# Kernel optimization log

Measured on AMD Instinct MI355X. Metric: run time of the kernel, lower is better.

The kernel has to match this reference:

```python
import jax, jax.numpy as jnp
import numpy as np

CAPS = 16          # num_capsules
DIM = 16           # capsule_dim
NUM_ROUTING = 3
L2_EPS = 1e-12     # tf.nn.l2_normalize epsilon


def setup_inputs() -> dict:
    key = jax.random.key(0)
    k1, k2 = jax.random.split(key)
    inputs = jax.random.normal(k1, (16, 64, 64, 128), dtype=jnp.float32)
    # Conv2D kernel, HWIO layout, fan-in scaled like glorot-ish init
    kernel = jax.random.normal(k2, (3, 3, 128, CAPS * DIM), dtype=jnp.float32) * 0.03
    bias = jnp.zeros((CAPS * DIM,), dtype=jnp.float32)
    return {"inputs": inputs, "kernel": kernel, "bias": bias}


def reference(inputs, kernel, bias):
    # Conv2D(caps*dim, 3x3, padding='same', activation='relu'), channels_last
    x = jax.lax.conv_general_dilated(
        inputs, kernel, window_strides=(1, 1), padding="SAME",
        dimension_numbers=("NHWC", "HWIO", "NHWC"))
    x = jax.nn.relu(x + bias)
    B, H, W, _ = x.shape
    x = x.reshape(B, H * W, CAPS, DIM)            # (B, N, C, D)
    b = jnp.zeros((B, H * W, CAPS), dtype=x.dtype)
    v = None
    for _ in range(NUM_ROUTING):
        c = jax.nn.softmax(b, axis=-1)             # over capsules
        s = jnp.einsum("bnc,bncd->bcd", c, x)      # weighted sum over spatial
        # tf.nn.l2_normalize along last axis
        v = s * jax.lax.rsqrt(jnp.maximum(jnp.sum(s * s, axis=-1, keepdims=True), L2_EPS))
        b = b + jnp.einsum("bncd,bcd->bnc", x, v)  # agreement update
    # tile v over spatial dims: (B,1,1,C*D) -> (B,H,W,C*D)
    out = jnp.broadcast_to(v.reshape(B, 1, 1, CAPS * DIM), (B, H, W, CAPS * DIM))
    return out
```

## Files before the change

### kernel.cpp

```cpp
#include <hip/hip_runtime.h>
#include <hip/hip_bf16.h>

typedef unsigned short u16;
typedef unsigned int   u32;

typedef __bf16 bf16x8 __attribute__((ext_vector_type(8)));
typedef float  f32x4  __attribute__((ext_vector_type(4)));

__device__ __forceinline__ u16 f2b(float f) {
    __hip_bfloat16 h = __float2bfloat16(f);
    u16 u; __builtin_memcpy(&u, &h, 2); return u;
}
__device__ __forceinline__ float blo(u32 u) { return __uint_as_float(u << 16); }
__device__ __forceinline__ float bhi(u32 u) { return __uint_as_float(u & 0xffff0000u); }

__global__ void k_prep(const float* __restrict__ wk,
                       u16* __restrict__ BF, float* __restrict__ stats) {
    int bx = blockIdx.x, tid = threadIdx.x;
    if (bx < 1152) {
        int t = bx * 256 + tid;
        int j  = t & 7;
        int n  = (t >> 3) & 255;
        int q  = (t >> 11) & 3;
        int kk = (t >> 13) & 3;
        int p  = t >> 15;
        BF[t] = f2b(wk[(p * 128 + kk * 32 + q * 8 + j) * 256 + n]);
    } else {
        stats[(bx - 1152) * 256 + tid] = 0.f;
    }
}

__launch_bounds__(256, 2)
__global__ void k_conv(const float* __restrict__ in, const u16* __restrict__ BF,
                       const float* __restrict__ bias,
                       u16* __restrict__ X, float* __restrict__ s0) {
    __shared__ u16 ldsA[12672];
    const int t = threadIdx.x;
    const int lane = t & 63, wid = t >> 6;
    const int q = lane >> 4, l15 = lane & 15;
    const int bb = blockIdx.x >> 6;
    const int h  = blockIdx.x & 63;
    const int wn0 = wid << 6;

#define STAGE(S) { \
    const int sb0 = wid * 396; \
    _Pragma("unroll") for (int i = 0; i < 7; ++i) { \
        int slot = sb0 + i * 64 + lane; \
        if (i < 6 || lane < 12) { \
            int pr = slot / 528; int rem = slot - pr * 528; \
            int wp = rem >> 3, cs = rem & 7; \
            int gc = (S) * 8 + (cs ^ (wp & 7)); \
            int y = h + pr - 1, x = wp - 1; \
            u16 ov[8]; \
            if (y >= 0 && y < 64 && x >= 0 && x < 64) { \
                const float4* s4 = (const float4*)(in + \
                    (((bb * 64 + y) * 64 + x) * 128 + gc * 8)); \
                float4 f0 = s4[0], f1 = s4[1]; \
                ov[0]=f2b(f0.x); ov[1]=f2b(f0.y); ov[2]=f2b(f0.z); ov[3]=f2b(f0.w); \
                ov[4]=f2b(f1.x); ov[5]=f2b(f1.y); ov[6]=f2b(f1.z); ov[7]=f2b(f1.w); \
            } else { \
                _Pragma("unroll") for (int j = 0; j < 8; ++j) ov[j] = 0; \
            } \
            uint4 wv; __builtin_memcpy(&wv, ov, 16); \
            *(uint4*)((char*)ldsA + slot * 16) = wv; \
        } \
    } }

#define LOADB(B, P, S) { \
    _Pragma("unroll") for (int kk = 0; kk < 2; ++kk) \
    _Pragma("unroll") for (int ni = 0; ni < 4; ++ni) \
        B[kk * 4 + ni] = *(const bf16x8*)(BFl + (P) * 32768 + \
                                          ((S) * 2 + kk) * 8192 + ni * 128); }

#define COMPP(B, DH, DW) { \
    _Pragma("unroll") for (int kk = 0; kk < 2; ++kk) { \
        bf16x8 af[4]; \
        _Pragma("unroll") for (int mi = 0; mi < 4; ++mi) { \
            int wp = mi * 16 + l15 + (DW); \
            int swz = (kk * 4 + q) ^ (wp & 7); \
            af[mi] = *(const bf16x8*)((const char*)ldsA + \
                (((DH) * 528 + wp * 8 + swz) << 4)); \
        } \
        _Pragma("unroll") for (int mi = 0; mi < 4; ++mi) \
        _Pragma("unroll") for (int ni = 0; ni < 4; ++ni) \
            acc[mi][ni] = __builtin_amdgcn_mfma_f32_16x16x32_bf16( \
                af[mi], B[kk * 4 + ni], acc[mi][ni], 0, 0, 0); } }

    const u16* BFl = BF + (q * 2048 + (wn0 + l15) * 8);

    f32x4 zero = {0.f, 0.f, 0.f, 0.f};
    f32x4 acc[4][4];
    #pragma unroll
    for (int mi = 0; mi < 4; ++mi)
        #pragma unroll
        for (int ni = 0; ni < 4; ++ni) acc[mi][ni] = zero;

    bf16x8 B0[8], B1[8];

    STAGE(0);
    __syncthreads();
    LOADB(B0, 0, 0);
    LOADB(B1, 1, 0); COMPP(B0, 0, 0);
    LOADB(B0, 2, 0); COMPP(B1, 0, 1);
    LOADB(B1, 3, 0); COMPP(B0, 0, 2);
    LOADB(B0, 4, 0); COMPP(B1, 1, 0);
    LOADB(B1, 5, 0); COMPP(B0, 1, 1);
    LOADB(B0, 6, 0); COMPP(B1, 1, 2);
    LOADB(B1, 7, 0); COMPP(B0, 2, 0);
    LOADB(B0, 8, 0); COMPP(B1, 2, 1);
    COMPP(B0, 2, 2);
    __syncthreads();

    STAGE(1);
    __syncthreads();
    LOADB(B0, 0, 1);
    LOADB(B1, 1, 1); COMPP(B0, 0, 0);
    LOADB(B0, 2, 1); COMPP(B1, 0, 1);
    LOADB(B1, 3, 1); COMPP(B0, 0, 2);
    LOADB(B0, 4, 1); COMPP(B1, 1, 0);
    LOADB(B1, 5, 1); COMPP(B0, 1, 1);
    LOADB(B0, 6, 1); COMPP(B1, 1, 2);
    LOADB(B1, 7, 1); COMPP(B0, 2, 0);
    LOADB(B0, 8, 1); COMPP(B1, 2, 1);
    COMPP(B0, 2, 2);

    float bv[4];
    #pragma unroll
    for (int ni = 0; ni < 4; ++ni) bv[ni] = bias[wn0 + ni * 16 + l15];
    float colsum[4] = {0.f, 0.f, 0.f, 0.f};
    u16* xrow = X + (((bb << 12) + (h << 6) + q * 4) * 256) + wn0 + l15;
    #pragma unroll
    for (int mi = 0; mi < 4; ++mi) {
        #pragma unroll
        for (int rr = 0; rr < 4; ++rr) {
            u16* xp = xrow + (mi * 16 + rr) * 256;
            #pragma unroll
            for (int ni = 0; ni < 4; ++ni) {
                float v = acc[mi][ni][rr] + bv[ni];
                v = v > 0.f ? v : 0.f;
                xp[ni * 16] = f2b(v);
                colsum[ni] += v;
            }
        }
    }
    #pragma unroll
    for (int ni = 0; ni < 4; ++ni) {
        float c = colsum[ni];
        c += __shfl_xor(c, 16);
        c += __shfl_xor(c, 32);
        if (lane < 16) atomicAdd(&s0[bb * 256 + wn0 + ni * 16 + l15], c);
    }
#undef STAGE
#undef LOADB
#undef COMPP
}

__launch_bounds__(256, 4)
__global__ void k_pass(const u16* __restrict__ X, const float* __restrict__ Sa,
                       const float* __restrict__ Sb, float* __restrict__ Sout,
                       int use2) {
    __shared__ float vs[272];
    __shared__ float red[4 * 272];
    const int t = threadIdx.x, b = blockIdx.y, chunk = blockIdx.x;
    const int c = t & 15, nl = t >> 4;
    const int lane = t & 63, wid = t >> 6;
    {
        float sa = Sa[b * 256 + t];
        float ss = sa * sa;
        #pragma unroll
        for (int off = 1; off < 16; off <<= 1) ss += __shfl_xor(ss, off);
        ss = ss < 1e-12f ? 1e-12f : ss;
        float vv = sa / sqrtf(ss);
        if (use2) {
            float sb = Sb[b * 256 + t];
            float s2v = sb * sb;
            #pragma unroll
            for (int off = 1; off < 16; off <<= 1) s2v += __shfl_xor(s2v, off);
            s2v = s2v < 1e-12f ? 1e-12f : s2v;
            vv += sb / sqrtf(s2v);
        }
        vs[(t >> 4) * 17 + (t & 15)] = vv;
    }
    const u16* xbase = X + ((b << 12) + chunk * 64 + nl) * 256 + c * 16;
    uint4 pa[8];
    #pragma unroll
    for (int r = 0; r < 4; ++r) {
        pa[2 * r]     = ((const uint4*)(xbase + r * 4096))[0];
        pa[2 * r + 1] = ((const uint4*)(xbase + r * 4096))[1];
    }
    __syncthreads();
    float vr[16];
    #pragma unroll
    for (int d = 0; d < 16; ++d) vr[d] = vs[c * 17 + d];

    float acc[16];
    #pragma unroll
    for (int d = 0; d < 16; ++d) acc[d] = 0.f;

    #pragma unroll
    for (int r = 0; r < 4; ++r) {
        u32 us[8];
        __builtin_memcpy(us, &pa[2 * r], 32);
        float xf[16];
        #pragma unroll
        for (int j = 0; j < 8; ++j) { xf[2*j] = blo(us[j]); xf[2*j+1] = bhi(us[j]); }
        float bvv = 0.f;
        #pragma unroll
        for (int d = 0; d < 16; ++d) bvv += xf[d] * vr[d];
        float e = __expf(bvv);
        float sm = e;
        #pragma unroll
        for (int off = 1; off < 16; off <<= 1) sm += __shfl_xor(sm, off);
        float w = e / sm;
        #pragma unroll
        for (int d = 0; d < 16; ++d) acc[d] += w * xf[d];
    }
    #pragma unroll
    for (int d = 0; d < 16; ++d) {
        acc[d] += __shfl_xor(acc[d], 16);
        acc[d] += __shfl_xor(acc[d], 32);
    }
    if (lane < 16) {
        #pragma unroll
        for (int d = 0; d < 16; ++d) red[wid * 272 + lane * 17 + d] = acc[d];
    }
    __syncthreads();
    {
        int c2 = t >> 4, d2 = t & 15;
        float tot = red[c2 * 17 + d2]       + red[272 + c2 * 17 + d2]
                  + red[544 + c2 * 17 + d2] + red[816 + c2 * 17 + d2];
        atomicAdd(&Sout[b * 256 + t], tot);
    }
}

__launch_bounds__(256, 4)
__global__ void k_bcast(const float* __restrict__ S, float* __restrict__ Out) {
    __shared__ float vls[256];
    int t = threadIdx.x, bx = blockIdx.x, b = blockIdx.y;
    float s = S[b * 256 + t];
    float ss = s * s;
    #pragma unroll
    for (int off = 1; off < 16; off <<= 1) ss += __shfl_xor(ss, off);
    ss = ss < 1e-12f ? 1e-12f : ss;
    vls[t] = s / sqrtf(ss);
    __syncthreads();
    float4 myv = ((const float4*)vls)[t & 63];
    float4* o = (float4*)Out + (long)b * 262144 + bx * 4096;
    #pragma unroll
    for (int j = 0; j < 16; ++j) o[j * 256 + t] = myv;
}

extern "C" void kernel_launch(void* const* d_in, const int* in_sizes, int n_in,
                              void* d_out, int out_size, void* d_ws, size_t ws_size,
                              hipStream_t stream) {
    const float* in   = (const float*)d_in[0];
    const float* wk   = (const float*)d_in[1];
    const float* bias = (const float*)d_in[2];
    float* out = (float*)d_out;
    char* ws = (char*)d_ws;

    const size_t OFF_BF  = 0;
    const size_t OFF_X   = 589824;
    const size_t OFF_ST  = 34144256;
    const size_t NEEDED  = OFF_ST + 3 * 16384;
    if (ws_size < NEEDED) return;

    u16* BF  = (u16*)(ws + OFF_BF);
    u16* X   = (u16*)(ws + OFF_X);
    float* s0 = (float*)(ws + OFF_ST);
    float* s2 = s0 + 4096;
    float* s3 = s2 + 4096;

    k_prep <<<1200, 256, 0, stream>>>(wk, BF, s0);
    k_conv <<<1024, 256, 0, stream>>>(in, BF, bias, X, s0);
    k_pass <<<dim3(64, 16), 256, 0, stream>>>(X, s0, s0, s2, 0);
    k_pass <<<dim3(64, 16), 256, 0, stream>>>(X, s0, s2, s3, 1);
    k_bcast<<<dim3(64, 16), 256, 0, stream>>>(s3, out);
}
```

Baseline: 159.9 us.

## Stage full 128-channel input halo in LDS once instead of two halves

The conv kernel now loads all 128 input channels of the 3-row halo into LDS in a single staging pass, doubling the LDS tile and widening the XOR swizzle to 16 chunks. This removes the second staging phase and two block barriers, and lets the B-fragment double-buffered MFMA chain run as one uninterrupted sequence of 18 steps. In exchange, LDS use per block doubles to about 50KB, which may limit how many blocks fit per CU, and all global loads now sit before compute with no overlap.

```diff
diff --git a/kernel.cpp b/kernel.cpp
--- a/kernel.cpp
+++ b/kernel.cpp
@@ -34,7 +34,7 @@
 __global__ void k_conv(const float* __restrict__ in, const u16* __restrict__ BF,
                        const float* __restrict__ bias,
                        u16* __restrict__ X, float* __restrict__ s0) {
-    __shared__ u16 ldsA[12672];
+    __shared__ u16 ldsA[25344];
     const int t = threadIdx.x;
     const int lane = t & 63, wid = t >> 6;
     const int q = lane >> 4, l15 = lane & 15;
@@ -42,29 +42,32 @@
     const int h  = blockIdx.x & 63;
     const int wn0 = wid << 6;
 
-#define STAGE(S) { \
-    const int sb0 = wid * 396; \
-    _Pragma("unroll") for (int i = 0; i < 7; ++i) { \
-        int slot = sb0 + i * 64 + lane; \
-        if (i < 6 || lane < 12) { \
-            int pr = slot / 528; int rem = slot - pr * 528; \
-            int wp = rem >> 3, cs = rem & 7; \
-            int gc = (S) * 8 + (cs ^ (wp & 7)); \
-            int y = h + pr - 1, x = wp - 1; \
-            u16 ov[8]; \
-            if (y >= 0 && y < 64 && x >= 0 && x < 64) { \
-                const float4* s4 = (const float4*)(in + \
-                    (((bb * 64 + y) * 64 + x) * 128 + gc * 8)); \
-                float4 f0 = s4[0], f1 = s4[1]; \
-                ov[0]=f2b(f0.x); ov[1]=f2b(f0.y); ov[2]=f2b(f0.z); ov[3]=f2b(f0.w); \
-                ov[4]=f2b(f1.x); ov[5]=f2b(f1.y); ov[6]=f2b(f1.z); ov[7]=f2b(f1.w); \
-            } else { \
-                _Pragma("unroll") for (int j = 0; j < 8; ++j) ov[j] = 0; \
-            } \
-            uint4 wv; __builtin_memcpy(&wv, ov, 16); \
-            *(uint4*)((char*)ldsA + slot * 16) = wv; \
-        } \
-    } }
+    {
+        const int sb0 = wid * 792;
+        #pragma unroll
+        for (int i = 0; i < 13; ++i) {
+            int slot = sb0 + i * 64 + lane;
+            if (i < 12 || lane < 24) {
+                int pr = slot / 1056; int rem = slot - pr * 1056;
+                int wp = rem >> 4, cs = rem & 15;
+                int gc = cs ^ (wp & 15);
+                int y = h + pr - 1, x = wp - 1;
+                u16 ov[8];
+                if (y >= 0 && y < 64 && x >= 0 && x < 64) {
+                    const float4* s4 = (const float4*)(in +
+                        (((bb * 64 + y) * 64 + x) * 128 + gc * 8));
+                    float4 f0 = s4[0], f1 = s4[1];
+                    ov[0]=f2b(f0.x); ov[1]=f2b(f0.y); ov[2]=f2b(f0.z); ov[3]=f2b(f0.w);
+                    ov[4]=f2b(f1.x); ov[5]=f2b(f1.y); ov[6]=f2b(f1.z); ov[7]=f2b(f1.w);
+                } else {
+                    #pragma unroll
+                    for (int j = 0; j < 8; ++j) ov[j] = 0;
+                }
+                uint4 wv; __builtin_memcpy(&wv, ov, 16);
+                *(uint4*)((char*)ldsA + slot * 16) = wv;
+            }
+        }
+    }
 
 #define LOADB(B, P, S) { \
     _Pragma("unroll") for (int kk = 0; kk < 2; ++kk) \
@@ -72,14 +75,15 @@
         B[kk * 4 + ni] = *(const bf16x8*)(BFl + (P) * 32768 + \
                                           ((S) * 2 + kk) * 8192 + ni * 128); }
 
-#define COMPP(B, DH, DW) { \
+#define COMPP(B, DH, DW, S) { \
     _Pragma("unroll") for (int kk = 0; kk < 2; ++kk) { \
         bf16x8 af[4]; \
         _Pragma("unroll") for (int mi = 0; mi < 4; ++mi) { \
             int wp = mi * 16 + l15 + (DW); \
-            int swz = (kk * 4 + q) ^ (wp & 7); \
+            int csc = (((S) * 2 + kk) << 2) + q; \
+            int swz = csc ^ (wp & 15); \
             af[mi] = *(const bf16x8*)((const char*)ldsA + \
-                (((DH) * 528 + wp * 8 + swz) << 4)); \
+                (((DH) * 1056 + wp * 16 + swz) << 4)); \
         } \
         _Pragma("unroll") for (int mi = 0; mi < 4; ++mi) \
         _Pragma("unroll") for (int ni = 0; ni < 4; ++ni) \
@@ -97,32 +101,26 @@
 
     bf16x8 B0[8], B1[8];
 
-    STAGE(0);
     __syncthreads();
     LOADB(B0, 0, 0);
-    LOADB(B1, 1, 0); COMPP(B0, 0, 0);
-    LOADB(B0, 2, 0); COMPP(B1, 0, 1);
-    LOADB(B1, 3, 0); COMPP(B0, 0, 2);
-    LOADB(B0, 4, 0); COMPP(B1, 1, 0);
-    LOADB(B1, 5, 0); COMPP(B0, 1, 1);
-    LOADB(B0, 6, 0); COMPP(B1, 1, 2);
-    LOADB(B1, 7, 0); COMPP(B0, 2, 0);
-    LOADB(B0, 8, 0); COMPP(B1, 2, 1);
-    COMPP(B0, 2, 2);
-    __syncthreads();
-
-    STAGE(1);
-    __syncthreads();
-    LOADB(B0, 0, 1);
-    LOADB(B1, 1, 1); COMPP(B0, 0, 0);
-    LOADB(B0, 2, 1); COMPP(B1, 0, 1);
-    LOADB(B1, 3, 1); COMPP(B0, 0, 2);
-    LOADB(B0, 4, 1); COMPP(B1, 1, 0);
-    LOADB(B1, 5, 1); COMPP(B0, 1, 1);
-    LOADB(B0, 6, 1); COMPP(B1, 1, 2);
-    LOADB(B1, 7, 1); COMPP(B0, 2, 0);
-    LOADB(B0, 8, 1); COMPP(B1, 2, 1);
-    COMPP(B0, 2, 2);
+    LOADB(B1, 0, 1); COMPP(B0, 0, 0, 0);
+    LOADB(B0, 1, 0); COMPP(B1, 0, 0, 1);
+    LOADB(B1, 1, 1); COMPP(B0, 0, 1, 0);
+    LOADB(B0, 2, 0); COMPP(B1, 0, 1, 1);
+    LOADB(B1, 2, 1); COMPP(B0, 0, 2, 0);
+    LOADB(B0, 3, 0); COMPP(B1, 0, 2, 1);
+    LOADB(B1, 3, 1); COMPP(B0, 1, 0, 0);
+    LOADB(B0, 4, 0); COMPP(B1, 1, 0, 1);
+    LOADB(B1, 4, 1); COMPP(B0, 1, 1, 0);
+    LOADB(B0, 5, 0); COMPP(B1, 1, 1, 1);
+    LOADB(B1, 5, 1); COMPP(B0, 1, 2, 0);
+    LOADB(B0, 6, 0); COMPP(B1, 1, 2, 1);
+    LOADB(B1, 6, 1); COMPP(B0, 2, 0, 0);
+    LOADB(B0, 7, 0); COMPP(B1, 2, 0, 1);
+    LOADB(B1, 7, 1); COMPP(B0, 2, 1, 0);
+    LOADB(B0, 8, 0); COMPP(B1, 2, 1, 1);
+    LOADB(B1, 8, 1); COMPP(B0, 2, 2, 0);
+    COMPP(B1, 2, 2, 1);
 
     float bv[4];
     #pragma unroll
@@ -150,7 +148,6 @@
         c += __shfl_xor(c, 32);
         if (lane < 16) atomicAdd(&s0[bb * 256 + wn0 + ni * 16 + l15], c);
     }
-#undef STAGE
 #undef LOADB
 #undef COMPP
 }
```

Result: no change. 162.0 us (+1.3%).
